# Kernel optimization log

Measured on AMD Instinct MI355X. Metric: run time of the kernel, lower is better.

## Reference

```python
import jax, jax.numpy as jnp
import numpy as np

def setup_inputs() -> dict:
    key = jax.random.key(0)
    k1, k2, k3 = jax.random.split(key, 3)
    N, G, D = 500000, 10000, 128
    n_embedding = jax.random.normal(k1, (N, D), dtype=jnp.float32)
    g_embedding = jax.random.normal(k2, (G, D), dtype=jnp.float32)
    n_batch = jnp.sort(jax.random.randint(k3, (N,), 0, G, dtype=jnp.int64))
    return {"n_embedding": n_embedding, "g_embedding": g_embedding,
            "n_batch": n_batch, "size": G}

def reference(n_embedding, g_embedding, n_batch, size):
    # gather graph embedding per node: [N, D]
    g_per_node = g_embedding[n_batch]
    # sigmoid of per-node dot product: [N]
    coefs = jax.nn.sigmoid(jnp.sum(n_embedding * g_per_node, axis=1))
    # weighted nodes scatter-added into per-graph pooled output: [G, D]
    weighted = coefs[:, None] * n_embedding
    return jax.ops.segment_sum(weighted, n_batch, num_segments=size)
```

## Files before the change

kernel.cpp:

```cpp
#include <hip/hip_runtime.h>
#include <math.h>


#define BLOCK_THREADS 256
#define GRID_BLOCKS   2048
#define U 8

__device__ __forceinline__ float dot4(float4 a, float4 b) {
    return a.x * b.x + a.y * b.y + a.z * b.z + a.w * b.w;
}

__global__ __launch_bounds__(BLOCK_THREADS)
void n2g_attention_kernel(const float* __restrict__ n_emb,
                          const float* __restrict__ g_emb,
                          const int*   __restrict__ n_batch,
                          float* __restrict__ out,
                          int N)
{
    const int hw_id  = blockIdx.x * (BLOCK_THREADS >> 5) + (threadIdx.x >> 5);
    const int l32    = threadIdx.x & 31;
    const int col    = l32 * 4;
    const int num_hw = GRID_BLOCKS * (BLOCK_THREADS >> 5);

    int per = (N + num_hw - 1) / num_hw;
    per = (per + U - 1) & ~(U - 1);
    const int start = hw_id * per;
    if (start >= N) return;
    const int end = min(start + per, N);

    float4 acc = make_float4(0.f, 0.f, 0.f, 0.f);
    int    cur_g = n_batch[start];
    float4 gv = *(const float4*)(g_emb + (size_t)cur_g * 128 + col);

    int i = start;
    for (; i + U <= end; i += U) {
        const int4 b0 = *(const int4*)(n_batch + i);
        const int4 b1 = *(const int4*)(n_batch + i + 4);

        float4 nv[U];
        #pragma unroll
        for (int j = 0; j < U; ++j)
            nv[j] = *(const float4*)(n_emb + (size_t)(i + j) * 128 + col);

        if (b1.w == cur_g) {
            float d[U];
            #pragma unroll
            for (int j = 0; j < U; ++j) d[j] = dot4(nv[j], gv);

            #pragma unroll
            for (int m = 1; m <= 16; m <<= 1) {
                #pragma unroll
                for (int j = 0; j < U; ++j) d[j] += __shfl_xor(d[j], m, 64);
            }

            #pragma unroll
            for (int j = 0; j < U; ++j) {
                const float c = 1.0f / (1.0f + __expf(-d[j]));
                acc.x += c * nv[j].x;
                acc.y += c * nv[j].y;
                acc.z += c * nv[j].z;
                acc.w += c * nv[j].w;
            }
        } else {
            const int b[U] = {b0.x, b0.y, b0.z, b0.w, b1.x, b1.y, b1.z, b1.w};
            #pragma unroll
            for (int j = 0; j < U; ++j) {
                if (b[j] != cur_g) {
                    atomicAdd(&out[(size_t)cur_g * 128 + col + 0], acc.x);
                    atomicAdd(&out[(size_t)cur_g * 128 + col + 1], acc.y);
                    atomicAdd(&out[(size_t)cur_g * 128 + col + 2], acc.z);
                    atomicAdd(&out[(size_t)cur_g * 128 + col + 3], acc.w);
                    acc = make_float4(0.f, 0.f, 0.f, 0.f);
                    cur_g = b[j];
                    gv = *(const float4*)(g_emb + (size_t)cur_g * 128 + col);
                }
                float d = dot4(nv[j], gv);
                #pragma unroll
                for (int m = 1; m <= 16; m <<= 1) d += __shfl_xor(d, m, 64);
                const float c = 1.0f / (1.0f + __expf(-d));
                acc.x += c * nv[j].x;
                acc.y += c * nv[j].y;
                acc.z += c * nv[j].z;
                acc.w += c * nv[j].w;
            }
        }
    }

    for (; i < end; ++i) {
        const int g = n_batch[i];
        if (g != cur_g) {
            atomicAdd(&out[(size_t)cur_g * 128 + col + 0], acc.x);
            atomicAdd(&out[(size_t)cur_g * 128 + col + 1], acc.y);
            atomicAdd(&out[(size_t)cur_g * 128 + col + 2], acc.z);
            atomicAdd(&out[(size_t)cur_g * 128 + col + 3], acc.w);
            acc = make_float4(0.f, 0.f, 0.f, 0.f);
            cur_g = g;
            gv = *(const float4*)(g_emb + (size_t)cur_g * 128 + col);
        }
        const float4 nv = *(const float4*)(n_emb + (size_t)i * 128 + col);
        float d = dot4(nv, gv);
        #pragma unroll
        for (int m = 1; m <= 16; m <<= 1) d += __shfl_xor(d, m, 64);
        const float c = 1.0f / (1.0f + __expf(-d));
        acc.x += c * nv.x;
        acc.y += c * nv.y;
        acc.z += c * nv.z;
        acc.w += c * nv.w;
    }

    atomicAdd(&out[(size_t)cur_g * 128 + col + 0], acc.x);
    atomicAdd(&out[(size_t)cur_g * 128 + col + 1], acc.y);
    atomicAdd(&out[(size_t)cur_g * 128 + col + 2], acc.z);
    atomicAdd(&out[(size_t)cur_g * 128 + col + 3], acc.w);
}

extern "C" void kernel_launch(void* const* d_in, const int* in_sizes, int n_in,
                              void* d_out, int out_size, void* d_ws, size_t ws_size,
                              hipStream_t stream) {
    const float* n_emb   = (const float*)d_in[0];
    const float* g_emb   = (const float*)d_in[1];
    const int*   n_batch = (const int*)d_in[2];
    float* out = (float*)d_out;
    const int N = in_sizes[2];

    hipMemsetAsync(d_out, 0, (size_t)out_size * sizeof(float), stream);

    n2g_attention_kernel<<<GRID_BLOCKS, BLOCK_THREADS, 0, stream>>>(
        n_emb, g_emb, n_batch, out, N);
}
```

Measured before the change: 355.3 us.

## Split fused attention pooling into separate coefficient and scatter kernels

The single fused kernel is split into two passes. The first computes per-node sigmoid coefficients with 8 lanes per node and writes them to workspace. The second re-reads the node embeddings and accumulates the coefficient-weighted rows into per-graph outputs with atomics. This removes the cross-lane dot-product reductions and exp work from the scatter loop. The cost is reading the 256MB node-embedding array twice plus an extra kernel launch, in a kernel that is already bandwidth bound.

```diff
diff --git a/kernel.cpp b/kernel.cpp
--- a/kernel.cpp
+++ b/kernel.cpp
@@ -2,116 +2,141 @@
 #include <math.h>
 
 
-#define BLOCK_THREADS 256
-#define GRID_BLOCKS   2048
-#define U 8
+#define BLOCKS 2048
+#define BT 256
 
 __device__ __forceinline__ float dot4(float4 a, float4 b) {
     return a.x * b.x + a.y * b.y + a.z * b.z + a.w * b.w;
 }
 
-__global__ __launch_bounds__(BLOCK_THREADS)
-void n2g_attention_kernel(const float* __restrict__ n_emb,
-                          const float* __restrict__ g_emb,
-                          const int*   __restrict__ n_batch,
-                          float* __restrict__ out,
-                          int N)
+__global__ __launch_bounds__(BT)
+void coef_kernel(const float* __restrict__ n_emb,
+                 const float* __restrict__ g_emb,
+                 const int*   __restrict__ n_batch,
+                 float* __restrict__ coefs,
+                 int N)
 {
-    const int hw_id  = blockIdx.x * (BLOCK_THREADS >> 5) + (threadIdx.x >> 5);
+    const int wave = blockIdx.x * (BT >> 6) + (threadIdx.x >> 6);
+    const int lane = threadIdx.x & 63;
+    const int oct  = lane >> 3;
+    const int l8   = lane & 7;
+    const int col  = l8 * 16;
+    const long num_waves = (long)BLOCKS * (BT >> 6);
+
+    for (long base = (long)wave * 16; base < N; base += num_waves * 16) {
+        const int nA = (int)min(base + oct,     (long)N - 1);
+        const int nB = (int)min(base + 8 + oct, (long)N - 1);
+
+        const int gA = n_batch[nA];
+        const int gB = n_batch[nB];
+
+        const float4* npA = (const float4*)(n_emb + (size_t)nA * 128 + col);
+        const float4* npB = (const float4*)(n_emb + (size_t)nB * 128 + col);
+        const float4* gpA = (const float4*)(g_emb + (size_t)gA * 128 + col);
+        const float4* gpB = (const float4*)(g_emb + (size_t)gB * 128 + col);
+
+        float4 nvA[4], nvB[4], gvA[4], gvB[4];
+        #pragma unroll
+        for (int t = 0; t < 4; ++t) { nvA[t] = npA[t]; nvB[t] = npB[t]; }
+        #pragma unroll
+        for (int t = 0; t < 4; ++t) { gvA[t] = gpA[t]; gvB[t] = gpB[t]; }
+
+        float dA = 0.f, dB = 0.f;
+        #pragma unroll
+        for (int t = 0; t < 4; ++t) { dA += dot4(nvA[t], gvA[t]); dB += dot4(nvB[t], gvB[t]); }
+
+        dA += __shfl_xor(dA, 1, 64);  dB += __shfl_xor(dB, 1, 64);
+        dA += __shfl_xor(dA, 2, 64);  dB += __shfl_xor(dB, 2, 64);
+        dA += __shfl_xor(dA, 4, 64);  dB += __shfl_xor(dB, 4, 64);
+
+        const float cA = 1.0f / (1.0f + __expf(-dA));
+        const float cB = 1.0f / (1.0f + __expf(-dB));
+
+        if (l8 == 0) {
+            if (base + oct     < N) coefs[nA] = cA;
+            if (base + 8 + oct < N) coefs[nB] = cB;
+        }
+    }
+}
+
+#define U 8
+
+#define FLUSH() do {                                              \
+    atomicAdd(&out[(size_t)cur_g * 128 + col + 0], acc.x);        \
+    atomicAdd(&out[(size_t)cur_g * 128 + col + 1], acc.y);        \
+    atomicAdd(&out[(size_t)cur_g * 128 + col + 2], acc.z);        \
+    atomicAdd(&out[(size_t)cur_g * 128 + col + 3], acc.w);        \
+    acc = make_float4(0.f, 0.f, 0.f, 0.f);                        \
+} while (0)
+
+__global__ __launch_bounds__(BT)
+void scatter_kernel(const float* __restrict__ n_emb,
+                    const float* __restrict__ coefs,
+                    const int*   __restrict__ n_batch,
+                    float* __restrict__ out,
+                    int N)
+{
+    const int hw_id  = blockIdx.x * (BT >> 5) + (threadIdx.x >> 5);
     const int l32    = threadIdx.x & 31;
     const int col    = l32 * 4;
-    const int num_hw = GRID_BLOCKS * (BLOCK_THREADS >> 5);
+    const int num_hw = BLOCKS * (BT >> 5);
 
     int per = (N + num_hw - 1) / num_hw;
-    per = (per + U - 1) & ~(U - 1);
+    per = (per + 2 * U - 1) & ~(2 * U - 1);
     const int start = hw_id * per;
     if (start >= N) return;
     const int end = min(start + per, N);
 
     float4 acc = make_float4(0.f, 0.f, 0.f, 0.f);
-    int    cur_g = n_batch[start];
-    float4 gv = *(const float4*)(g_emb + (size_t)cur_g * 128 + col);
+    int cur_g = n_batch[start];
 
     int i = start;
     for (; i + U <= end; i += U) {
-        const int4 b0 = *(const int4*)(n_batch + i);
-        const int4 b1 = *(const int4*)(n_batch + i + 4);
+        const int4   b0 = *(const int4*)(n_batch + i);
+        const int4   b1 = *(const int4*)(n_batch + i + 4);
+        const float4 c0 = *(const float4*)(coefs + i);
+        const float4 c1 = *(const float4*)(coefs + i + 4);
 
         float4 nv[U];
         #pragma unroll
         for (int j = 0; j < U; ++j)
             nv[j] = *(const float4*)(n_emb + (size_t)(i + j) * 128 + col);
 
+        const float cc[U] = {c0.x, c0.y, c0.z, c0.w, c1.x, c1.y, c1.z, c1.w};
+
         if (b1.w == cur_g) {
-            float d[U];
-            #pragma unroll
-            for (int j = 0; j < U; ++j) d[j] = dot4(nv[j], gv);
-
-            #pragma unroll
-            for (int m = 1; m <= 16; m <<= 1) {
-                #pragma unroll
-                for (int j = 0; j < U; ++j) d[j] += __shfl_xor(d[j], m, 64);
-            }
-
             #pragma unroll
             for (int j = 0; j < U; ++j) {
-                const float c = 1.0f / (1.0f + __expf(-d[j]));
-                acc.x += c * nv[j].x;
-                acc.y += c * nv[j].y;
-                acc.z += c * nv[j].z;
-                acc.w += c * nv[j].w;
+                acc.x += cc[j] * nv[j].x;
+                acc.y += cc[j] * nv[j].y;
+                acc.z += cc[j] * nv[j].z;
+                acc.w += cc[j] * nv[j].w;
             }
         } else {
-            const int b[U] = {b0.x, b0.y, b0.z, b0.w, b1.x, b1.y, b1.z, b1.w};
+            const int bb[U] = {b0.x, b0.y, b0.z, b0.w, b1.x, b1.y, b1.z, b1.w};
             #pragma unroll
             for (int j = 0; j < U; ++j) {
-                if (b[j] != cur_g) {
-                    atomicAdd(&out[(size_t)cur_g * 128 + col + 0], acc.x);
-                    atomicAdd(&out[(size_t)cur_g * 128 + col + 1], acc.y);
-                    atomicAdd(&out[(size_t)cur_g * 128 + col + 2], acc.z);
-                    atomicAdd(&out[(size_t)cur_g * 128 + col + 3], acc.w);
-                    acc = make_float4(0.f, 0.f, 0.f, 0.f);
-                    cur_g = b[j];
-                    gv = *(const float4*)(g_emb + (size_t)cur_g * 128 + col);
-                }
-                float d = dot4(nv[j], gv);
-                #pragma unroll
-                for (int m = 1; m <= 16; m <<= 1) d += __shfl_xor(d, m, 64);
-                const float c = 1.0f / (1.0f + __expf(-d));
-                acc.x += c * nv[j].x;
-                acc.y += c * nv[j].y;
-                acc.z += c * nv[j].z;
-                acc.w += c * nv[j].w;
+                if (bb[j] != cur_g) { FLUSH(); cur_g = bb[j]; }
+                acc.x += cc[j] * nv[j].x;
+                acc.y += cc[j] * nv[j].y;
+                acc.z += cc[j] * nv[j].z;
+                acc.w += cc[j] * nv[j].w;
             }
         }
     }
 
     for (; i < end; ++i) {
         const int g = n_batch[i];
-        if (g != cur_g) {
-            atomicAdd(&out[(size_t)cur_g * 128 + col + 0], acc.x);
-            atomicAdd(&out[(size_t)cur_g * 128 + col + 1], acc.y);
-            atomicAdd(&out[(size_t)cur_g * 128 + col + 2], acc.z);
-            atomicAdd(&out[(size_t)cur_g * 128 + col + 3], acc.w);
-            acc = make_float4(0.f, 0.f, 0.f, 0.f);
-            cur_g = g;
-            gv = *(const float4*)(g_emb + (size_t)cur_g * 128 + col);
-        }
+        const float c = coefs[i];
         const float4 nv = *(const float4*)(n_emb + (size_t)i * 128 + col);
-        float d = dot4(nv, gv);
-        #pragma unroll
-        for (int m = 1; m <= 16; m <<= 1) d += __shfl_xor(d, m, 64);
-        const float c = 1.0f / (1.0f + __expf(-d));
+        if (g != cur_g) { FLUSH(); cur_g = g; }
         acc.x += c * nv.x;
         acc.y += c * nv.y;
         acc.z += c * nv.z;
         acc.w += c * nv.w;
     }
 
-    atomicAdd(&out[(size_t)cur_g * 128 + col + 0], acc.x);
-    atomicAdd(&out[(size_t)cur_g * 128 + col + 1], acc.y);
-    atomicAdd(&out[(size_t)cur_g * 128 + col + 2], acc.z);
-    atomicAdd(&out[(size_t)cur_g * 128 + col + 3], acc.w);
+    FLUSH();
 }
 
 extern "C" void kernel_launch(void* const* d_in, const int* in_sizes, int n_in,
@@ -120,11 +145,12 @@
     const float* n_emb   = (const float*)d_in[0];
     const float* g_emb   = (const float*)d_in[1];
     const int*   n_batch = (const int*)d_in[2];
-    float* out = (float*)d_out;
+    float* out   = (float*)d_out;
+    float* coefs = (float*)d_ws;
     const int N = in_sizes[2];
 
     hipMemsetAsync(d_out, 0, (size_t)out_size * sizeof(float), stream);
 
-    n2g_attention_kernel<<<GRID_BLOCKS, BLOCK_THREADS, 0, stream>>>(
-        n_emb, g_emb, n_batch, out, N);
+    coef_kernel<<<BLOCKS, BT, 0, stream>>>(n_emb, g_emb, n_batch, coefs, N);
+    scatter_kernel<<<BLOCKS, BT, 0, stream>>>(n_emb, coefs, n_batch, out, N);
 }
```

Result: slower. 410.5 us (+15.5%).
